# Kernel optimization log

Hardware: AMD Instinct MI355X
Metric: run time of the kernel (lower is better)

The kernel has to match this reference:

```python
import jax, jax.numpy as jnp
import numpy as np

N_NODES = 50000
N_EDGES = 800000
D_IN = 512
D_OUT = 512


def setup_inputs() -> dict:
    key = jax.random.key(0)
    k1, k2, k3, k4, k5 = jax.random.split(key, 5)
    x = jax.random.normal(k1, (N_NODES, D_IN), dtype=jnp.float32)
    weight = jax.random.normal(k2, (D_IN, D_OUT), dtype=jnp.float32) * (1.0 / np.sqrt(D_IN))
    edge_weight = jax.random.uniform(k3, (N_EDGES,), dtype=jnp.float32)
    edge_src = jax.random.randint(k4, (N_EDGES,), 0, N_NODES, dtype=jnp.int32)
    edge_dst = jax.random.randint(k5, (N_EDGES,), 0, N_NODES, dtype=jnp.int32)
    return {"x": x, "weight": weight, "edge_weight": edge_weight,
            "edge_src": edge_src, "edge_dst": edge_dst}


def reference(x, weight, edge_weight, edge_src, edge_dst):
    # support = x @ W  (dense GEMM, [N, D_out])
    support = jnp.matmul(x, weight)
    # output = adj @ support  (SpMM in COO form):
    # gather source rows, scale by edge weight, scatter-add into destinations
    msgs = support[edge_src] * edge_weight[:, None]          # [E, D_out]
    output = jax.ops.segment_sum(msgs, edge_dst, num_segments=N_NODES)
    return output
```

## Files before the change

kernel.cpp:

```cpp
#include <hip/hip_runtime.h>
#include <stdint.h>

#define N_NODES 50000
#define N_EDGES 800000
#define D 512
#define M_PAD 50048
#define SCAN_NB 196

typedef __attribute__((ext_vector_type(8))) __bf16 bf16x8;
typedef __attribute__((ext_vector_type(4))) float f32x4;

static __device__ __forceinline__ unsigned short f2bf(float f) {
  unsigned u = __float_as_uint(f);
  u += 0x7fff + ((u >> 16) & 1);
  return (unsigned short)(u >> 16);
}
static __device__ __forceinline__ float bf2f(unsigned short h) {
  return __uint_as_float(((unsigned)h) << 16);
}

static __device__ __forceinline__ void gload_lds16(const void* g, void* l) {
  __builtin_amdgcn_global_load_lds((const __attribute__((address_space(1))) unsigned*)g,
                                   (__attribute__((address_space(3))) unsigned*)l, 16, 0, 0);
}

__global__ void k_cvt_x(const float* __restrict__ x, unsigned short* __restrict__ xb) {
  long long base = ((long long)blockIdx.x * blockDim.x + threadIdx.x) * 4;
  if (base >= (long long)M_PAD * D) return;
  int row = (int)(base >> 9);
  ushort4 o;
  if (row < N_NODES) {
    float4 v = *(const float4*)(x + base);
    o.x = f2bf(v.x); o.y = f2bf(v.y); o.z = f2bf(v.z); o.w = f2bf(v.w);
  } else {
    o.x = 0; o.y = 0; o.z = 0; o.w = 0;
  }
  *(ushort4*)(xb + base) = o;
}

__global__ void k_cvt_wt(const float* __restrict__ w, unsigned short* __restrict__ wt) {
  int k = blockIdx.x;
  int n = threadIdx.x;
  wt[n * D + k] = f2bf(w[k * D + n]);
}

__global__ __launch_bounds__(256) void k_gemm(const unsigned short* __restrict__ A,
                                              const unsigned short* __restrict__ Bt,
                                              unsigned short* __restrict__ C) {
  __shared__ unsigned short lds_a[128 * 32];
  __shared__ unsigned short lds_b[128 * 32];
  const int tid  = threadIdx.x;
  const int bm   = blockIdx.x >> 2;
  const int bn   = blockIdx.x & 3;
  const int m0   = bm * 128, n0 = bn * 128;
  const int wave = tid >> 6, lane = tid & 63;
  const int wm   = wave & 1, wn = wave >> 1;
  const int l15  = lane & 15, quad = lane >> 4;

  f32x4 acc[4][4];
#pragma unroll
  for (int i = 0; i < 4; i++)
#pragma unroll
    for (int j = 0; j < 4; j++) acc[i][j] = f32x4{0.f, 0.f, 0.f, 0.f};

  for (int kt = 0; kt < D / 32; ++kt) {
    const int k0 = kt * 32;
    __syncthreads();
#pragma unroll
    for (int c = 0; c < 2; c++) {
      int i = c * 256 + wave * 64 + lane;
      int r = i >> 2, kc = (i & 3) << 3;
      gload_lds16(&A[(long long)(m0 + r) * D + k0 + kc], &lds_a[(c * 256 + wave * 64) * 8]);
      gload_lds16(&Bt[(long long)(n0 + r) * D + k0 + kc], &lds_b[(c * 256 + wave * 64) * 8]);
    }
    __syncthreads();
    bf16x8 af[4], bfr[4];
#pragma unroll
    for (int t = 0; t < 4; t++) {
      af[t]  = *(const bf16x8*)&lds_a[(wm * 64 + t * 16 + l15) * 32 + quad * 8];
      bfr[t] = *(const bf16x8*)&lds_b[(wn * 64 + t * 16 + l15) * 32 + quad * 8];
    }
#pragma unroll
    for (int i = 0; i < 4; i++)
#pragma unroll
      for (int j = 0; j < 4; j++)
        acc[i][j] = __builtin_amdgcn_mfma_f32_16x16x32_bf16(af[i], bfr[j], acc[i][j], 0, 0, 0);
  }
#pragma unroll
  for (int i = 0; i < 4; i++)
#pragma unroll
    for (int j = 0; j < 4; j++)
#pragma unroll
      for (int r = 0; r < 4; r++) {
        int row = m0 + wm * 64 + i * 16 + quad * 4 + r;
        int col = n0 + wn * 64 + j * 16 + l15;
        C[(long long)row * D + col] = f2bf(acc[i][j][r]);
      }
}

__global__ void k_zero(int* deg) {
  int i = blockIdx.x * 256 + threadIdx.x;
  if (i < N_NODES) deg[i] = 0;
}
__global__ void k_hist(const int* __restrict__ dst, int* deg) {
  int e = blockIdx.x * 256 + threadIdx.x;
  if (e < N_EDGES) atomicAdd(&deg[dst[e]], 1);
}

__global__ void k_scan1(const int* __restrict__ deg, int* __restrict__ bsum) {
  __shared__ int red[256];
  int i = blockIdx.x * 256 + threadIdx.x;
  red[threadIdx.x] = (i < N_NODES) ? deg[i] : 0;
  __syncthreads();
#pragma unroll
  for (int s = 128; s > 0; s >>= 1) {
    if ((int)threadIdx.x < s) red[threadIdx.x] += red[threadIdx.x + s];
    __syncthreads();
  }
  if (threadIdx.x == 0) bsum[blockIdx.x] = red[0];
}
__global__ void k_scan2(int* __restrict__ bsum) {
  __shared__ int tmp[256];
  int t = threadIdx.x;
  int v = (t < SCAN_NB) ? bsum[t] : 0;
  tmp[t] = v;
  __syncthreads();
#pragma unroll
  for (int s = 1; s < 256; s <<= 1) {
    int add = (t >= s) ? tmp[t - s] : 0;
    __syncthreads();
    tmp[t] += add;
    __syncthreads();
  }
  if (t < SCAN_NB) bsum[t] = tmp[t] - v;
}
__global__ void k_scan3(const int* __restrict__ deg, const int* __restrict__ bsum,
                        int* __restrict__ off, int* __restrict__ cur) {
  __shared__ int tmp[256];
  int t = threadIdx.x, i = blockIdx.x * 256 + t;
  int v = (i < N_NODES) ? deg[i] : 0;
  tmp[t] = v;
  __syncthreads();
#pragma unroll
  for (int s = 1; s < 256; s <<= 1) {
    int add = (t >= s) ? tmp[t - s] : 0;
    __syncthreads();
    tmp[t] += add;
    __syncthreads();
  }
  int pre = tmp[t] - v + bsum[blockIdx.x];
  if (i < N_NODES) {
    off[i] = pre;
    cur[i] = pre;
    if (i == N_NODES - 1) off[N_NODES] = pre + v;
  }
}

__global__ void k_fill(const int* __restrict__ src, const int* __restrict__ dst,
                       const float* __restrict__ w, int* cur,
                       int* __restrict__ csrc, float* __restrict__ cw) {
  int e = blockIdx.x * 256 + threadIdx.x;
  if (e >= N_EDGES) return;
  int d = dst[e];
  int p = atomicAdd(&cur[d], 1);
  csrc[p] = src[e];
  cw[p]   = w[e];
}

__global__ __launch_bounds__(256) void k_agg(const int* __restrict__ off, const int* __restrict__ csrc,
                                             const float* __restrict__ cw,
                                             const unsigned short* __restrict__ S,
                                             float* __restrict__ out) {
  __shared__ float s_part[4 * 512];
  const int node  = blockIdx.x;
  const int start = off[node], end = off[node + 1];
  const int wave  = threadIdx.x >> 6, lane = threadIdx.x & 63;
  float a[8];
#pragma unroll
  for (int k = 0; k < 8; k++) a[k] = 0.f;

#define EDGE_FMA(V, W)                                             \
  do {                                                             \
    a[0] = fmaf(W, bf2f((unsigned short)(V.x & 0xffffu)), a[0]);   \
    a[1] = fmaf(W, bf2f((unsigned short)(V.x >> 16)),     a[1]);   \
    a[2] = fmaf(W, bf2f((unsigned short)(V.y & 0xffffu)), a[2]);   \
    a[3] = fmaf(W, bf2f((unsigned short)(V.y >> 16)),     a[3]);   \
    a[4] = fmaf(W, bf2f((unsigned short)(V.z & 0xffffu)), a[4]);   \
    a[5] = fmaf(W, bf2f((unsigned short)(V.z >> 16)),     a[5]);   \
    a[6] = fmaf(W, bf2f((unsigned short)(V.w & 0xffffu)), a[6]);   \
    a[7] = fmaf(W, bf2f((unsigned short)(V.w >> 16)),     a[7]);   \
  } while (0)

  int e = start + wave;
  for (; e + 4 < end; e += 8) {
    int   s0 = csrc[e],     s1 = csrc[e + 4];
    float w0 = cw[e],       w1 = cw[e + 4];
    uint4 v0 = *(const uint4*)(S + (size_t)s0 * D + lane * 8);
    uint4 v1 = *(const uint4*)(S + (size_t)s1 * D + lane * 8);
    EDGE_FMA(v0, w0);
    EDGE_FMA(v1, w1);
  }
  if (e < end) {
    int   s0 = csrc[e];
    float w0 = cw[e];
    uint4 v0 = *(const uint4*)(S + (size_t)s0 * D + lane * 8);
    EDGE_FMA(v0, w0);
  }
#undef EDGE_FMA

  float4* sp = (float4*)&s_part[wave * 512 + lane * 8];
  sp[0] = make_float4(a[0], a[1], a[2], a[3]);
  sp[1] = make_float4(a[4], a[5], a[6], a[7]);
  __syncthreads();
  int col = threadIdx.x * 2;
  float2 r0 = *(const float2*)&s_part[0 * 512 + col];
  float2 r1 = *(const float2*)&s_part[1 * 512 + col];
  float2 r2 = *(const float2*)&s_part[2 * 512 + col];
  float2 r3 = *(const float2*)&s_part[3 * 512 + col];
  *(float2*)(out + (size_t)node * D + col) =
      make_float2(r0.x + r1.x + r2.x + r3.x, r0.y + r1.y + r2.y + r3.y);
}

extern "C" void kernel_launch(void* const* d_in, const int* in_sizes, int n_in,
                              void* d_out, int out_size, void* d_ws, size_t ws_size,
                              hipStream_t stream) {
  const float* x    = (const float*)d_in[0];
  const float* w    = (const float*)d_in[1];
  const float* ew   = (const float*)d_in[2];
  const int*   esrc = (const int*)d_in[3];
  const int*   edst = (const int*)d_in[4];
  float* out = (float*)d_out;

  char* p = (char*)d_ws;
  auto align256 = [](size_t v) { return (v + 255) & ~(size_t)255; };
  unsigned short* xb = (unsigned short*)p;  p += align256((size_t)M_PAD * D * 2);
  unsigned short* sb = (unsigned short*)p;  p += align256((size_t)M_PAD * D * 2);
  unsigned short* wt = (unsigned short*)p;  p += align256((size_t)D * D * 2);
  int*   deg  = (int*)p;   p += align256((size_t)N_NODES * 4);
  int*   off  = (int*)p;   p += align256((size_t)(N_NODES + 1) * 4);
  int*   cur  = (int*)p;   p += align256((size_t)N_NODES * 4);
  int*   csrc = (int*)p;   p += align256((size_t)N_EDGES * 4);
  float* cw   = (float*)p; p += align256((size_t)N_EDGES * 4);
  int*   bsum = (int*)p;   p += align256((size_t)256 * 4);

  k_cvt_x<<<(M_PAD * D / 4 + 255) / 256, 256, 0, stream>>>(x, xb);
  k_cvt_wt<<<D, D, 0, stream>>>(w, wt);
  k_gemm<<<391 * 4, 256, 0, stream>>>(xb, wt, sb);
  k_zero<<<(N_NODES + 255) / 256, 256, 0, stream>>>(deg);
  k_hist<<<(N_EDGES + 255) / 256, 256, 0, stream>>>(edst, deg);
  k_scan1<<<SCAN_NB, 256, 0, stream>>>(deg, bsum);
  k_scan2<<<1, 256, 0, stream>>>(bsum);
  k_scan3<<<SCAN_NB, 256, 0, stream>>>(deg, bsum, off, cur);
  k_fill<<<(N_EDGES + 255) / 256, 256, 0, stream>>>(esrc, edst, ew, cur, csrc, cw);
  k_agg<<<N_NODES, 256, 0, stream>>>(off, csrc, cw, sb, out);
}
```

Baseline: 437.2 us.

## Fuse conversion and CSR build into cooperative kernel; one wave per node aggregation

Merges the x/W conversion, degree histogram, three scan kernels and the CSR fill into one cooperative kernel separated by grid-wide syncs, which removes several kernel launches. The aggregation kernel now gives each wave its own destination node. Each wave loads up to 64 edge indices and weights in parallel and broadcasts them with shuffles, issuing four row gathers per iteration. This drops the LDS cross-wave reduction and the block sync. The cooperative kernel needs all 1024 blocks co-resident and serialises phases through grid syncs, and the conversion now uses a grid-stride loop over fewer threads.

```diff
diff --git a/kernel.cpp b/kernel.cpp
--- a/kernel.cpp
+++ b/kernel.cpp
@@ -1,11 +1,15 @@
 #include <hip/hip_runtime.h>
+#include <hip/hip_cooperative_groups.h>
 #include <stdint.h>
+
+namespace cg = cooperative_groups;
 
 #define N_NODES 50000
 #define N_EDGES 800000
 #define D 512
 #define M_PAD 50048
 #define SCAN_NB 196
+#define CSR_BLOCKS 1024
 
 typedef __attribute__((ext_vector_type(8))) __bf16 bf16x8;
 typedef __attribute__((ext_vector_type(4))) float f32x4;
@@ -24,24 +28,103 @@
                                    (__attribute__((address_space(3))) unsigned*)l, 16, 0, 0);
 }
 
-__global__ void k_cvt_x(const float* __restrict__ x, unsigned short* __restrict__ xb) {
-  long long base = ((long long)blockIdx.x * blockDim.x + threadIdx.x) * 4;
-  if (base >= (long long)M_PAD * D) return;
-  int row = (int)(base >> 9);
-  ushort4 o;
-  if (row < N_NODES) {
-    float4 v = *(const float4*)(x + base);
-    o.x = f2bf(v.x); o.y = f2bf(v.y); o.z = f2bf(v.z); o.w = f2bf(v.w);
-  } else {
-    o.x = 0; o.y = 0; o.z = 0; o.w = 0;
-  }
-  *(ushort4*)(xb + base) = o;
-}
-
-__global__ void k_cvt_wt(const float* __restrict__ w, unsigned short* __restrict__ wt) {
-  int k = blockIdx.x;
-  int n = threadIdx.x;
-  wt[n * D + k] = f2bf(w[k * D + n]);
+__global__ __launch_bounds__(256) void k_csr(const float* __restrict__ x,
+                                             const float* __restrict__ w,
+                                             unsigned short* __restrict__ xb,
+                                             unsigned short* __restrict__ wt,
+                                             const int* __restrict__ esrc,
+                                             const int* __restrict__ edst,
+                                             const float* __restrict__ ew,
+                                             int* __restrict__ deg,
+                                             int* __restrict__ off,
+                                             int* __restrict__ cur,
+                                             int* __restrict__ csrc,
+                                             float* __restrict__ cw,
+                                             int* __restrict__ bsum) {
+  cg::grid_group grid = cg::this_grid();
+  __shared__ int red[256];
+  const int gtid = blockIdx.x * 256 + threadIdx.x;
+  const int gsz  = gridDim.x * 256;
+
+  const int nchunk = M_PAD * D / 4;
+  for (int i = gtid; i < nchunk; i += gsz) {
+    long long base = (long long)i * 4;
+    int row = (int)(base >> 9);
+    ushort4 o;
+    if (row < N_NODES) {
+      float4 v = *(const float4*)(x + base);
+      o.x = f2bf(v.x); o.y = f2bf(v.y); o.z = f2bf(v.z); o.w = f2bf(v.w);
+    } else {
+      o.x = 0; o.y = 0; o.z = 0; o.w = 0;
+    }
+    *(ushort4*)(xb + base) = o;
+  }
+  for (int i = gtid; i < D * D; i += gsz) {
+    int k = i >> 9, n = i & 511;
+    wt[n * D + k] = f2bf(w[i]);
+  }
+  for (int i = gtid; i < N_NODES; i += gsz) deg[i] = 0;
+  grid.sync();
+
+  for (int e = gtid; e < N_EDGES; e += gsz) atomicAdd(&deg[edst[e]], 1);
+  grid.sync();
+
+  if (blockIdx.x < SCAN_NB) {
+    int i = blockIdx.x * 256 + threadIdx.x;
+    red[threadIdx.x] = (i < N_NODES) ? deg[i] : 0;
+    __syncthreads();
+#pragma unroll
+    for (int s = 128; s > 0; s >>= 1) {
+      if ((int)threadIdx.x < s) red[threadIdx.x] += red[threadIdx.x + s];
+      __syncthreads();
+    }
+    if (threadIdx.x == 0) bsum[blockIdx.x] = red[0];
+  }
+  grid.sync();
+
+  if (blockIdx.x == 0) {
+    int t = threadIdx.x;
+    int v = (t < SCAN_NB) ? bsum[t] : 0;
+    red[t] = v;
+    __syncthreads();
+#pragma unroll
+    for (int s = 1; s < 256; s <<= 1) {
+      int add = (t >= s) ? red[t - s] : 0;
+      __syncthreads();
+      red[t] += add;
+      __syncthreads();
+    }
+    if (t < SCAN_NB) bsum[t] = red[t] - v;
+  }
+  grid.sync();
+
+  if (blockIdx.x < SCAN_NB) {
+    int t = threadIdx.x, i = blockIdx.x * 256 + t;
+    int v = (i < N_NODES) ? deg[i] : 0;
+    red[t] = v;
+    __syncthreads();
+#pragma unroll
+    for (int s = 1; s < 256; s <<= 1) {
+      int add = (t >= s) ? red[t - s] : 0;
+      __syncthreads();
+      red[t] += add;
+      __syncthreads();
+    }
+    int pre = red[t] - v + bsum[blockIdx.x];
+    if (i < N_NODES) {
+      off[i] = pre;
+      cur[i] = pre;
+      if (i == N_NODES - 1) off[N_NODES] = pre + v;
+    }
+  }
+  grid.sync();
+
+  for (int e = gtid; e < N_EDGES; e += gsz) {
+    int d = edst[e];
+    int p = atomicAdd(&cur[d], 1);
+    csrc[p] = esrc[e];
+    cw[p]   = ew[e];
+  }
 }
 
 __global__ __launch_bounds__(256) void k_gemm(const unsigned short* __restrict__ A,
@@ -98,127 +181,60 @@
       }
 }
 
-__global__ void k_zero(int* deg) {
-  int i = blockIdx.x * 256 + threadIdx.x;
-  if (i < N_NODES) deg[i] = 0;
-}
-__global__ void k_hist(const int* __restrict__ dst, int* deg) {
-  int e = blockIdx.x * 256 + threadIdx.x;
-  if (e < N_EDGES) atomicAdd(&deg[dst[e]], 1);
-}
-
-__global__ void k_scan1(const int* __restrict__ deg, int* __restrict__ bsum) {
-  __shared__ int red[256];
-  int i = blockIdx.x * 256 + threadIdx.x;
-  red[threadIdx.x] = (i < N_NODES) ? deg[i] : 0;
-  __syncthreads();
-#pragma unroll
-  for (int s = 128; s > 0; s >>= 1) {
-    if ((int)threadIdx.x < s) red[threadIdx.x] += red[threadIdx.x + s];
-    __syncthreads();
-  }
-  if (threadIdx.x == 0) bsum[blockIdx.x] = red[0];
-}
-__global__ void k_scan2(int* __restrict__ bsum) {
-  __shared__ int tmp[256];
-  int t = threadIdx.x;
-  int v = (t < SCAN_NB) ? bsum[t] : 0;
-  tmp[t] = v;
-  __syncthreads();
-#pragma unroll
-  for (int s = 1; s < 256; s <<= 1) {
-    int add = (t >= s) ? tmp[t - s] : 0;
-    __syncthreads();
-    tmp[t] += add;
-    __syncthreads();
-  }
-  if (t < SCAN_NB) bsum[t] = tmp[t] - v;
-}
-__global__ void k_scan3(const int* __restrict__ deg, const int* __restrict__ bsum,
-                        int* __restrict__ off, int* __restrict__ cur) {
-  __shared__ int tmp[256];
-  int t = threadIdx.x, i = blockIdx.x * 256 + t;
-  int v = (i < N_NODES) ? deg[i] : 0;
-  tmp[t] = v;
-  __syncthreads();
-#pragma unroll
-  for (int s = 1; s < 256; s <<= 1) {
-    int add = (t >= s) ? tmp[t - s] : 0;
-    __syncthreads();
-    tmp[t] += add;
-    __syncthreads();
-  }
-  int pre = tmp[t] - v + bsum[blockIdx.x];
-  if (i < N_NODES) {
-    off[i] = pre;
-    cur[i] = pre;
-    if (i == N_NODES - 1) off[N_NODES] = pre + v;
-  }
-}
-
-__global__ void k_fill(const int* __restrict__ src, const int* __restrict__ dst,
-                       const float* __restrict__ w, int* cur,
-                       int* __restrict__ csrc, float* __restrict__ cw) {
-  int e = blockIdx.x * 256 + threadIdx.x;
-  if (e >= N_EDGES) return;
-  int d = dst[e];
-  int p = atomicAdd(&cur[d], 1);
-  csrc[p] = src[e];
-  cw[p]   = w[e];
-}
-
-__global__ __launch_bounds__(256) void k_agg(const int* __restrict__ off, const int* __restrict__ csrc,
+static __device__ __forceinline__ void edge_fma(float (&a)[8], uint4 v, float w) {
+  a[0] = fmaf(w, bf2f((unsigned short)(v.x & 0xffffu)), a[0]);
+  a[1] = fmaf(w, bf2f((unsigned short)(v.x >> 16)),     a[1]);
+  a[2] = fmaf(w, bf2f((unsigned short)(v.y & 0xffffu)), a[2]);
+  a[3] = fmaf(w, bf2f((unsigned short)(v.y >> 16)),     a[3]);
+  a[4] = fmaf(w, bf2f((unsigned short)(v.z & 0xffffu)), a[4]);
+  a[5] = fmaf(w, bf2f((unsigned short)(v.z >> 16)),     a[5]);
+  a[6] = fmaf(w, bf2f((unsigned short)(v.w & 0xffffu)), a[6]);
+  a[7] = fmaf(w, bf2f((unsigned short)(v.w >> 16)),     a[7]);
+}
+
+__global__ __launch_bounds__(256) void k_agg(const int* __restrict__ off,
+                                             const int* __restrict__ csrc,
                                              const float* __restrict__ cw,
                                              const unsigned short* __restrict__ S,
                                              float* __restrict__ out) {
-  __shared__ float s_part[4 * 512];
-  const int node  = blockIdx.x;
+  const int wave = threadIdx.x >> 6, lane = threadIdx.x & 63;
+  const int node = blockIdx.x * 4 + wave;
+  if (node >= N_NODES) return;
   const int start = off[node], end = off[node + 1];
-  const int wave  = threadIdx.x >> 6, lane = threadIdx.x & 63;
   float a[8];
 #pragma unroll
   for (int k = 0; k < 8; k++) a[k] = 0.f;
 
-#define EDGE_FMA(V, W)                                             \
-  do {                                                             \
-    a[0] = fmaf(W, bf2f((unsigned short)(V.x & 0xffffu)), a[0]);   \
-    a[1] = fmaf(W, bf2f((unsigned short)(V.x >> 16)),     a[1]);   \
-    a[2] = fmaf(W, bf2f((unsigned short)(V.y & 0xffffu)), a[2]);   \
-    a[3] = fmaf(W, bf2f((unsigned short)(V.y >> 16)),     a[3]);   \
-    a[4] = fmaf(W, bf2f((unsigned short)(V.z & 0xffffu)), a[4]);   \
-    a[5] = fmaf(W, bf2f((unsigned short)(V.z >> 16)),     a[5]);   \
-    a[6] = fmaf(W, bf2f((unsigned short)(V.w & 0xffffu)), a[6]);   \
-    a[7] = fmaf(W, bf2f((unsigned short)(V.w >> 16)),     a[7]);   \
-  } while (0)
-
-  int e = start + wave;
-  for (; e + 4 < end; e += 8) {
-    int   s0 = csrc[e],     s1 = csrc[e + 4];
-    float w0 = cw[e],       w1 = cw[e + 4];
-    uint4 v0 = *(const uint4*)(S + (size_t)s0 * D + lane * 8);
-    uint4 v1 = *(const uint4*)(S + (size_t)s1 * D + lane * 8);
-    EDGE_FMA(v0, w0);
-    EDGE_FMA(v1, w1);
-  }
-  if (e < end) {
-    int   s0 = csrc[e];
-    float w0 = cw[e];
-    uint4 v0 = *(const uint4*)(S + (size_t)s0 * D + lane * 8);
-    EDGE_FMA(v0, w0);
-  }
-#undef EDGE_FMA
-
-  float4* sp = (float4*)&s_part[wave * 512 + lane * 8];
-  sp[0] = make_float4(a[0], a[1], a[2], a[3]);
-  sp[1] = make_float4(a[4], a[5], a[6], a[7]);
-  __syncthreads();
-  int col = threadIdx.x * 2;
-  float2 r0 = *(const float2*)&s_part[0 * 512 + col];
-  float2 r1 = *(const float2*)&s_part[1 * 512 + col];
-  float2 r2 = *(const float2*)&s_part[2 * 512 + col];
-  float2 r3 = *(const float2*)&s_part[3 * 512 + col];
-  *(float2*)(out + (size_t)node * D + col) =
-      make_float2(r0.x + r1.x + r2.x + r3.x, r0.y + r1.y + r2.y + r3.y);
+  for (int base = start; base < end; base += 64) {
+    int m = end - base; if (m > 64) m = 64;
+    int   c  = 0;
+    float wv = 0.f;
+    if (lane < m) { c = csrc[base + lane]; wv = cw[base + lane]; }
+    int j = 0;
+    for (; j + 4 <= m; j += 4) {
+      int   s0 = __shfl(c, j),      s1 = __shfl(c, j + 1);
+      int   s2 = __shfl(c, j + 2),  s3 = __shfl(c, j + 3);
+      float w0 = __shfl(wv, j),     w1 = __shfl(wv, j + 1);
+      float w2 = __shfl(wv, j + 2), w3 = __shfl(wv, j + 3);
+      uint4 v0 = *(const uint4*)(S + (size_t)s0 * D + lane * 8);
+      uint4 v1 = *(const uint4*)(S + (size_t)s1 * D + lane * 8);
+      uint4 v2 = *(const uint4*)(S + (size_t)s2 * D + lane * 8);
+      uint4 v3 = *(const uint4*)(S + (size_t)s3 * D + lane * 8);
+      edge_fma(a, v0, w0);
+      edge_fma(a, v1, w1);
+      edge_fma(a, v2, w2);
+      edge_fma(a, v3, w3);
+    }
+    for (; j < m; j++) {
+      int   s0 = __shfl(c, j);
+      float w0 = __shfl(wv, j);
+      uint4 v0 = *(const uint4*)(S + (size_t)s0 * D + lane * 8);
+      edge_fma(a, v0, w0);
+    }
+  }
+  float4* o = (float4*)(out + (size_t)node * D + lane * 8);
+  o[0] = make_float4(a[0], a[1], a[2], a[3]);
+  o[1] = make_float4(a[4], a[5], a[6], a[7]);
 }
 
 extern "C" void kernel_launch(void* const* d_in, const int* in_sizes, int n_in,
@@ -243,14 +259,11 @@
   float* cw   = (float*)p; p += align256((size_t)N_EDGES * 4);
   int*   bsum = (int*)p;   p += align256((size_t)256 * 4);
 
-  k_cvt_x<<<(M_PAD * D / 4 + 255) / 256, 256, 0, stream>>>(x, xb);
-  k_cvt_wt<<<D, D, 0, stream>>>(w, wt);
+  void* args[] = { (void*)&x, (void*)&w, (void*)&xb, (void*)&wt,
+                   (void*)&esrc, (void*)&edst, (void*)&ew,
+                   (void*)&deg, (void*)&off, (void*)&cur,
+                   (void*)&csrc, (void*)&cw, (void*)&bsum };
+  hipLaunchCooperativeKernel((void*)k_csr, dim3(CSR_BLOCKS), dim3(256), args, 0, stream);
   k_gemm<<<391 * 4, 256, 0, stream>>>(xb, wt, sb);
-  k_zero<<<(N_NODES + 255) / 256, 256, 0, stream>>>(deg);
-  k_hist<<<(N_EDGES + 255) / 256, 256, 0, stream>>>(edst, deg);
-  k_scan1<<<SCAN_NB, 256, 0, stream>>>(deg, bsum);
-  k_scan2<<<1, 256, 0, stream>>>(bsum);
-  k_scan3<<<SCAN_NB, 256, 0, stream>>>(deg, bsum, off, cur);
-  k_fill<<<(N_EDGES + 255) / 256, 256, 0, stream>>>(esrc, edst, ew, cur, csrc, cw);
-  k_agg<<<N_NODES, 256, 0, stream>>>(off, csrc, cw, sb, out);
-}
+  k_agg<<<N_NODES / 4, 256, 0, stream>>>(off, csrc, cw, sb, out);
+}
```

After: 964.1 us. 2.21x slower.
